# Optimization experiments

Hardware: AMD Instinct MI355X
Metric: run time of the kernel (lower is better)

Reference implementation:

```python
import jax, jax.numpy as jnp
import numpy as np

N = 100000
E = 500000
F_IN = 128
HID = 64
HEADS = 4
OUT = 32
NEG_SLOPE = 0.2


def _glorot(key, shape):
    fan_in, fan_out = shape[0], shape[1]
    lim = jnp.sqrt(6.0 / (fan_in + fan_out))
    return jax.random.uniform(key, shape, jnp.float32, -lim, lim)


def setup_inputs() -> dict:
    key = jax.random.key(0)
    ks = jax.random.split(key, 20)
    x = jax.random.normal(ks[0], (N, F_IN), jnp.float32)
    edge_index = jax.random.randint(ks[1], (2, E), 0, N, jnp.int64)
    edge_attr = jax.random.uniform(ks[2], (E, 1), jnp.float32)
    d1 = HEADS * HID
    params = {
        # conv1: F_IN -> HEADS x HID
        "Wl1": _glorot(ks[3], (F_IN, d1)), "bl1": jnp.zeros((d1,), jnp.float32),
        "Wr1": _glorot(ks[4], (F_IN, d1)), "br1": jnp.zeros((d1,), jnp.float32),
        "We1": _glorot(ks[5], (1, d1)),
        "att1": _glorot(ks[6], (HEADS, HID)),
        "b1": jnp.zeros((d1,), jnp.float32),
        "Wl2": _glorot(ks[7], (d1, OUT)), "bl2": jnp.zeros((OUT,), jnp.float32),
        "Wr2": _glorot(ks[8], (d1, OUT)), "br2": jnp.zeros((OUT,), jnp.float32),
        "We2": _glorot(ks[9], (1, OUT)),
        "att2": _glorot(ks[10], (1, OUT)),
        "b2": jnp.zeros((OUT,), jnp.float32),
    }
    return {"x": x, "edge_index": edge_index, "edge_attr": edge_attr, **params}


def gatv2_conv(x, src, dst, edge_attr, Wl, bl, Wr, br, We, att, bias, heads, out_ch):
    """PyG GATv2Conv (add_self_loops=False, concat=True, share_weights=False)."""
    n = x.shape[0]
    xl = (x @ Wl + bl).reshape(n, heads, out_ch)          # source transform
    xr = (x @ Wr + br).reshape(n, heads, out_ch)          # target transform
    e = (edge_attr @ We).reshape(-1, heads, out_ch)       # [E, H, C]
    m = jax.nn.leaky_relu(xl[src] + xr[dst] + e, NEG_SLOPE)  # [E, H, C]
    alpha = jnp.einsum('ehc,hc->eh', m, att)              # [E, H]
    # softmax over edges sharing the same destination node
    amax = jax.ops.segment_max(alpha, dst, num_segments=n)
    ealpha = jnp.exp(alpha - amax[dst])
    denom = jax.ops.segment_sum(ealpha, dst, num_segments=n)
    alpha = ealpha / (denom[dst] + 1e-16)
    out = jax.ops.segment_sum(xl[src] * alpha[:, :, None], dst, num_segments=n)
    return out.reshape(n, heads * out_ch) + bias


def reference(x, edge_index, edge_attr, Wl1, bl1, Wr1, br1, We1, att1, b1,
              Wl2, bl2, Wr2, br2, We2, att2, b2):
    src, dst = edge_index[0], edge_index[1]
    h = gatv2_conv(x, src, dst, edge_attr, Wl1, bl1, Wr1, br1, We1, att1, b1, HEADS, HID)
    h = jax.nn.relu(h)  # dropout is identity at inference
    out = gatv2_conv(h, src, dst, edge_attr, Wl2, bl2, Wr2, br2, We2, att2, b2, 1, OUT)
    return out
```

## Files before the change

### kernel.cpp

```cpp
#include <hip/hip_runtime.h>
#include <cstddef>
#include <cstdint>

#define F_IN 128
#define D1   256
#define HEADS 4
#define HID   64
#define OUT_C 32
#define NEG   0.2f

typedef unsigned short ushort_t;
typedef __attribute__((ext_vector_type(8))) short short8;
typedef __attribute__((ext_vector_type(4))) float f32x4;
typedef __attribute__((ext_vector_type(4))) unsigned short ushort4v;

__device__ __forceinline__ float bu2f(ushort_t u) {
  return __uint_as_float(((unsigned)u) << 16);
}
__device__ __forceinline__ ushort_t f2bu(float f) {
  unsigned u = __float_as_uint(f);
  return (ushort_t)((u + 0x7FFF + ((u >> 16) & 1)) >> 16);
}

__global__ void cvt_x_k(const float* __restrict__ x, ushort_t* __restrict__ xb, int total4) {
  int i = blockIdx.x * blockDim.x + threadIdx.x;
  if (i >= total4) return;
  f32x4 v = ((const f32x4*)x)[i];
  ushort4v o;
  o[0] = f2bu(v[0]); o[1] = f2bu(v[1]); o[2] = f2bu(v[2]); o[3] = f2bu(v[3]);
  *(ushort4v*)(xb + 4 * (size_t)i) = o;
}

__global__ void prep_b1_k(const float* __restrict__ Wl, const float* __restrict__ Wr,
                          const float* __restrict__ bl, const float* __restrict__ br,
                          ushort_t* __restrict__ Bt, float* __restrict__ biasc) {
  int i = blockIdx.x * blockDim.x + threadIdx.x;
  int nn = i >> 7, k = i & 127;
  float v = (nn < D1) ? Wl[(size_t)k * D1 + nn] : Wr[(size_t)k * D1 + (nn - D1)];
  Bt[(size_t)nn * F_IN + k] = f2bu(v);
  if (k == 0) biasc[nn] = (nn < D1) ? bl[nn] : br[nn - D1];
}

__global__ void prep_b2_k(const float* __restrict__ Wl, const float* __restrict__ Wr,
                          const float* __restrict__ bl, const float* __restrict__ br,
                          ushort_t* __restrict__ Bt, float* __restrict__ biasc) {
  int i = blockIdx.x * blockDim.x + threadIdx.x;
  int nn = i >> 8, k = i & 255;
  float v = (nn < OUT_C) ? Wl[(size_t)k * OUT_C + nn] : Wr[(size_t)k * OUT_C + (nn - OUT_C)];
  Bt[(size_t)nn * D1 + k] = f2bu(v);
  if (k == 0) biasc[nn] = (nn < OUT_C) ? bl[nn] : br[nn - OUT_C];
}

template <int WM, int WN, int BK>
__global__ void mfma_gemm(const ushort_t* __restrict__ A, const ushort_t* __restrict__ Bt,
                          const float* __restrict__ biasc, ushort_t* __restrict__ C,
                          int M, int N, int K) {
  constexpr int BM = WM * 64, BN = WN * 64;
  constexpr int LD = BK + 8;
  constexpr int CPR = BK / 8;
  __shared__ ushort_t As[BM][LD];
  __shared__ ushort_t Bs[BN][LD];
  const int tid = threadIdx.x;
  const int wave = tid >> 6, lane = tid & 63;
  const int wm = wave % WM, wn = wave / WM;
  const int quad = lane >> 4, l16 = lane & 15;
  const int m0 = blockIdx.x * BM, n0 = blockIdx.y * BN;
  const int nth = WM * WN * 64;
  f32x4 acc[4][4] = {};
  for (int k0 = 0; k0 < K; k0 += BK) {
    for (int i = tid; i < BM * CPR; i += nth) {
      int r = i / CPR, ch = i % CPR;
      int gr = m0 + r;
      short8 v = {};
      if (gr < M) v = *(const short8*)(A + (size_t)gr * K + k0 + ch * 8);
      *(short8*)(&As[r][ch * 8]) = v;
    }
    for (int i = tid; i < BN * CPR; i += nth) {
      int r = i / CPR, ch = i % CPR;
      short8 v = {};
      if (n0 + r < N) v = *(const short8*)(Bt + (size_t)(n0 + r) * K + k0 + ch * 8);
      *(short8*)(&Bs[r][ch * 8]) = v;
    }
    __syncthreads();
#pragma unroll
    for (int ks = 0; ks < BK; ks += 32) {
      short8 af[4], bfr[4];
#pragma unroll
      for (int mi = 0; mi < 4; ++mi)
        af[mi] = *(const short8*)(&As[wm * 64 + mi * 16 + l16][ks + quad * 8]);
#pragma unroll
      for (int ni = 0; ni < 4; ++ni)
        bfr[ni] = *(const short8*)(&Bs[wn * 64 + ni * 16 + l16][ks + quad * 8]);
#pragma unroll
      for (int mi = 0; mi < 4; ++mi)
#pragma unroll
        for (int ni = 0; ni < 4; ++ni)
          acc[mi][ni] = __builtin_amdgcn_mfma_f32_16x16x32_bf16(af[mi], bfr[ni],
                                                                acc[mi][ni], 0, 0, 0);
    }
    __syncthreads();
  }
#pragma unroll
  for (int mi = 0; mi < 4; ++mi) {
#pragma unroll
    for (int r = 0; r < 4; ++r) {
      int grow = m0 + wm * 64 + mi * 16 + quad * 4 + r;
      if (grow >= M) continue;
#pragma unroll
      for (int ni = 0; ni < 4; ++ni) {
        int gcol = n0 + wn * 64 + ni * 16 + l16;
        C[(size_t)grow * N + gcol] = f2bu(acc[mi][ni][r] + biasc[gcol]);
      }
    }
  }
}

__global__ void hist_k(const int* __restrict__ dst, int* __restrict__ deg, int e) {
  int i = blockIdx.x * blockDim.x + threadIdx.x;
  if (i < e) atomicAdd(&deg[dst[i]], 1);
}

__global__ void scan_block_k(const int* __restrict__ deg, int* __restrict__ row_ptr,
                             int* __restrict__ bsum, int n) {
  __shared__ int s[1024];
  int i = blockIdx.x * 1024 + threadIdx.x;
  int v = (i < n) ? deg[i] : 0;
  s[threadIdx.x] = v;
  __syncthreads();
  for (int off = 1; off < 1024; off <<= 1) {
    int t = (threadIdx.x >= off) ? s[threadIdx.x - off] : 0;
    __syncthreads();
    s[threadIdx.x] += t;
    __syncthreads();
  }
  if (i < n) row_ptr[i + 1] = s[threadIdx.x];
  if (threadIdx.x == 1023) bsum[blockIdx.x] = s[1023];
}

__global__ void scan_bsum_k(int* __restrict__ bsum, int nb) {
  __shared__ int s[128];
  int v = (threadIdx.x < nb) ? bsum[threadIdx.x] : 0;
  s[threadIdx.x] = v;
  __syncthreads();
  for (int off = 1; off < 128; off <<= 1) {
    int t = (threadIdx.x >= off) ? s[threadIdx.x - off] : 0;
    __syncthreads();
    s[threadIdx.x] += t;
    __syncthreads();
  }
  if (threadIdx.x < nb) bsum[threadIdx.x] = s[threadIdx.x] - v;
}

__global__ void add_off_k(int* __restrict__ row_ptr, const int* __restrict__ bsum, int n) {
  int i = blockIdx.x * blockDim.x + threadIdx.x;
  if (i == 0) row_ptr[0] = 0;
  if (i < n) row_ptr[i + 1] += bsum[i >> 10];
}

__global__ void copy_cursor_k(const int* __restrict__ row_ptr, int* __restrict__ cursor, int n) {
  int i = blockIdx.x * blockDim.x + threadIdx.x;
  if (i < n) cursor[i] = row_ptr[i];
}

__global__ void fill_k(const int* __restrict__ src, const int* __restrict__ dst,
                       const float* __restrict__ eattr, int* __restrict__ cursor,
                       int* __restrict__ csr_src, float* __restrict__ csr_w, int e) {
  int i = blockIdx.x * blockDim.x + threadIdx.x;
  if (i >= e) return;
  int p = atomicAdd(&cursor[dst[i]], 1);
  csr_src[p] = src[i];
  csr_w[p]   = eattr[i];
}

__global__ void gat1_k(const int* __restrict__ row_ptr, const int* __restrict__ csr_src,
                       const float* __restrict__ csr_w, const ushort_t* __restrict__ C1,
                       const float* __restrict__ We, const float* __restrict__ att,
                       const float* __restrict__ bias, ushort_t* __restrict__ h1, int n) {
  int node = (int)(((size_t)blockIdx.x * blockDim.x + threadIdx.x) >> 6);
  int lane = threadIdx.x & 63;
  if (node >= n) return;
  int cb = lane * 4;
  ushort4v xr4 = *(const ushort4v*)(C1 + (size_t)node * 512 + 256 + cb);
  float xrr[4], Wev[4], attv[4], acc[4] = {0.f, 0.f, 0.f, 0.f};
  float esum = 0.f;
#pragma unroll
  for (int j = 0; j < 4; ++j) {
    xrr[j] = bu2f(xr4[j]);
    Wev[j] = We[cb + j];
    attv[j] = att[cb + j];
  }
  int p1 = row_ptr[node + 1];
  for (int p = row_ptr[node]; p < p1; ++p) {
    int s = csr_src[p];
    float wgt = csr_w[p];
    ushort4v xl4 = *(const ushort4v*)(C1 + (size_t)s * 512 + cb);
    float xv[4], v = 0.f;
#pragma unroll
    for (int j = 0; j < 4; ++j) {
      xv[j] = bu2f(xl4[j]);
      float m = xv[j] + xrr[j] + wgt * Wev[j];
      m = m > 0.f ? m : NEG * m;
      v += m * attv[j];
    }
    v += __shfl_xor(v, 1, 64);
    v += __shfl_xor(v, 2, 64);
    v += __shfl_xor(v, 4, 64);
    v += __shfl_xor(v, 8, 64);
    float eh = __expf(v);
    esum += eh;
#pragma unroll
    for (int j = 0; j < 4; ++j) acc[j] += eh * xv[j];
  }
  float inv = 1.f / (esum + 1e-16f);
  ushort4v o;
#pragma unroll
  for (int j = 0; j < 4; ++j) {
    float t = acc[j] * inv + bias[cb + j];
    o[j] = f2bu(t > 0.f ? t : 0.f);
  }
  *(ushort4v*)(h1 + (size_t)node * D1 + cb) = o;
}

__global__ void gat2_k(const int* __restrict__ row_ptr, const int* __restrict__ csr_src,
                       const float* __restrict__ csr_w, const ushort_t* __restrict__ C2,
                       const float* __restrict__ We, const float* __restrict__ att,
                       const float* __restrict__ bias, float* __restrict__ out, int n) {
  size_t t = (size_t)blockIdx.x * blockDim.x + threadIdx.x;
  int node = (int)(t >> 3);
  int g = (int)(t & 7);
  if (node >= n) return;
  int cb = g * 4;
  ushort4v xr4 = *(const ushort4v*)(C2 + (size_t)node * 64 + 32 + cb);
  float xrr[4], Wev[4], attv[4], acc[4] = {0.f, 0.f, 0.f, 0.f};
  float esum = 0.f;
#pragma unroll
  for (int j = 0; j < 4; ++j) {
    xrr[j] = bu2f(xr4[j]);
    Wev[j] = We[cb + j];
    attv[j] = att[cb + j];
  }
  int p1 = row_ptr[node + 1];
  for (int p = row_ptr[node]; p < p1; ++p) {
    int s = csr_src[p];
    float wgt = csr_w[p];
    ushort4v xl4 = *(const ushort4v*)(C2 + (size_t)s * 64 + cb);
    float xv[4], v = 0.f;
#pragma unroll
    for (int j = 0; j < 4; ++j) {
      xv[j] = bu2f(xl4[j]);
      float m = xv[j] + xrr[j] + wgt * Wev[j];
      m = m > 0.f ? m : NEG * m;
      v += m * attv[j];
    }
    v += __shfl_xor(v, 1, 64);
    v += __shfl_xor(v, 2, 64);
    v += __shfl_xor(v, 4, 64);
    float eh = __expf(v);
    esum += eh;
#pragma unroll
    for (int j = 0; j < 4; ++j) acc[j] += eh * xv[j];
  }
  float inv = 1.f / (esum + 1e-16f);
  f32x4 ov;
#pragma unroll
  for (int j = 0; j < 4; ++j) ov[j] = acc[j] * inv + bias[cb + j];
  *(f32x4*)(out + (size_t)node * OUT_C + cb) = ov;
}

extern "C" void kernel_launch(void* const* d_in, const int* in_sizes, int n_in,
                              void* d_out, int out_size, void* d_ws, size_t ws_size,
                              hipStream_t stream) {
  const float* x     = (const float*)d_in[0];
  const int*   eidx  = (const int*)d_in[1];
  const float* eattr = (const float*)d_in[2];
  const float* Wl1 = (const float*)d_in[3];
  const float* bl1 = (const float*)d_in[4];
  const float* Wr1 = (const float*)d_in[5];
  const float* br1 = (const float*)d_in[6];
  const float* We1 = (const float*)d_in[7];
  const float* att1 = (const float*)d_in[8];
  const float* b1  = (const float*)d_in[9];
  const float* Wl2 = (const float*)d_in[10];
  const float* bl2 = (const float*)d_in[11];
  const float* Wr2 = (const float*)d_in[12];
  const float* br2 = (const float*)d_in[13];
  const float* We2 = (const float*)d_in[14];
  const float* att2 = (const float*)d_in[15];
  const float* b2  = (const float*)d_in[16];

  const int n = in_sizes[0] / F_IN;
  const int e = in_sizes[2];
  const int* src = eidx;
  const int* dst = eidx + e;
  float* out = (float*)d_out;

  char* w = (char*)d_ws;
  ushort_t* x_bf = (ushort_t*)w;  w += (size_t)n * F_IN * 2;
  ushort_t* C1   = (ushort_t*)w;  w += (size_t)n * 512 * 2;
  ushort_t* h1b  = (ushort_t*)w;  w += (size_t)n * D1 * 2;
  ushort_t* C2   = (ushort_t*)w;  w += (size_t)n * 64 * 2;
  ushort_t* Bt1  = (ushort_t*)w;  w += 512 * F_IN * 2;
  ushort_t* Bt2  = (ushort_t*)w;  w += 64 * D1 * 2;
  float* bias1c  = (float*)w;     w += 512 * 4;
  float* bias2c  = (float*)w;     w += 64 * 4;
  float* csr_w   = (float*)w;     w += (size_t)e * 4;
  int*   csr_src = (int*)w;       w += (size_t)e * 4;
  int*   row_ptr = (int*)w;       w += ((size_t)n + 1) * 4;
  int*   cursor  = (int*)w;       w += (size_t)n * 4;
  int*   bsum    = (int*)w;       w += 512;
  int*   deg = cursor;

  dim3 blk(256);
  const int nb = (n + 1023) / 1024;

  cvt_x_k<<<(n * F_IN / 4 + 255) / 256, blk, 0, stream>>>(x, x_bf, n * F_IN / 4);
  prep_b1_k<<<(512 * 128) / 256, blk, 0, stream>>>(Wl1, Wr1, bl1, br1, Bt1, bias1c);
  prep_b2_k<<<(64 * 256) / 256, blk, 0, stream>>>(Wl2, Wr2, bl2, br2, Bt2, bias2c);

  hipMemsetAsync(deg, 0, (size_t)n * sizeof(int), stream);
  hist_k<<<(e + 255) / 256, blk, 0, stream>>>(dst, deg, e);
  scan_block_k<<<nb, 1024, 0, stream>>>(deg, row_ptr, bsum, n);
  scan_bsum_k<<<1, 128, 0, stream>>>(bsum, nb);
  add_off_k<<<(n + 255) / 256, blk, 0, stream>>>(row_ptr, bsum, n);
  copy_cursor_k<<<(n + 255) / 256, blk, 0, stream>>>(row_ptr, cursor, n);
  fill_k<<<(e + 255) / 256, blk, 0, stream>>>(src, dst, eattr, cursor, csr_src, csr_w, e);

  mfma_gemm<2, 2, 64><<<dim3((n + 127) / 128, 4), blk, 0, stream>>>(
      x_bf, Bt1, bias1c, C1, n, 512, F_IN);
  gat1_k<<<(n + 3) / 4, blk, 0, stream>>>(row_ptr, csr_src, csr_w, C1,
                                          We1, att1, b1, h1b, n);

  mfma_gemm<4, 1, 64><<<dim3((n + 255) / 256, 1), blk, 0, stream>>>(
      h1b, Bt2, bias2c, C2, n, 64, D1);
  gat2_k<<<((size_t)n * 8 + 255) / 256, blk, 0, stream>>>(row_ptr, csr_src, csr_w, C2,
                                                          We2, att2, b2, out, n);
}
```

Before: 382.9 us.

## Fuse x conversion into GEMM, pack CSR edges, unroll gather loops, retile GEMM2

Removes the separate fp32-to-bf16 conversion kernel by converting x on the fly while loading A tiles in the first GEMM. CSR source index and edge weight are packed into a single int2 array, so each edge needs one load instead of two. The attention aggregation loops in both GAT kernels are unrolled by four to keep more independent gathers in flight. The second GEMM moves to 128-thread blocks of 128 rows for more blocks. The first GEMM now reads fp32 x, and with four column blocks per row tile it re-reads and re-converts x each time.

```diff
diff --git a/kernel.cpp b/kernel.cpp
--- a/kernel.cpp
+++ b/kernel.cpp
@@ -22,15 +22,6 @@
   return (ushort_t)((u + 0x7FFF + ((u >> 16) & 1)) >> 16);
 }
 
-__global__ void cvt_x_k(const float* __restrict__ x, ushort_t* __restrict__ xb, int total4) {
-  int i = blockIdx.x * blockDim.x + threadIdx.x;
-  if (i >= total4) return;
-  f32x4 v = ((const f32x4*)x)[i];
-  ushort4v o;
-  o[0] = f2bu(v[0]); o[1] = f2bu(v[1]); o[2] = f2bu(v[2]); o[3] = f2bu(v[3]);
-  *(ushort4v*)(xb + 4 * (size_t)i) = o;
-}
-
 __global__ void prep_b1_k(const float* __restrict__ Wl, const float* __restrict__ Wr,
                           const float* __restrict__ bl, const float* __restrict__ br,
                           ushort_t* __restrict__ Bt, float* __restrict__ biasc) {
@@ -51,8 +42,8 @@
   if (k == 0) biasc[nn] = (nn < OUT_C) ? bl[nn] : br[nn - OUT_C];
 }
 
-template <int WM, int WN, int BK>
-__global__ void mfma_gemm(const ushort_t* __restrict__ A, const ushort_t* __restrict__ Bt,
+template <int WM, int WN, int BK, bool CVT>
+__global__ void mfma_gemm(const void* __restrict__ Av, const ushort_t* __restrict__ Bt,
                           const float* __restrict__ biasc, ushort_t* __restrict__ C,
                           int M, int N, int K) {
   constexpr int BM = WM * 64, BN = WN * 64;
@@ -71,9 +62,26 @@
     for (int i = tid; i < BM * CPR; i += nth) {
       int r = i / CPR, ch = i % CPR;
       int gr = m0 + r;
-      short8 v = {};
-      if (gr < M) v = *(const short8*)(A + (size_t)gr * K + k0 + ch * 8);
-      *(short8*)(&As[r][ch * 8]) = v;
+      if (CVT) {
+        const float* A32 = (const float*)Av;
+        f32x4 v0 = {}, v1 = {};
+        if (gr < M) {
+          const float* p = A32 + (size_t)gr * K + k0 + ch * 8;
+          v0 = *(const f32x4*)p;
+          v1 = *(const f32x4*)(p + 4);
+        }
+        short8 o;
+        o[0] = (short)f2bu(v0[0]); o[1] = (short)f2bu(v0[1]);
+        o[2] = (short)f2bu(v0[2]); o[3] = (short)f2bu(v0[3]);
+        o[4] = (short)f2bu(v1[0]); o[5] = (short)f2bu(v1[1]);
+        o[6] = (short)f2bu(v1[2]); o[7] = (short)f2bu(v1[3]);
+        *(short8*)(&As[r][ch * 8]) = o;
+      } else {
+        const ushort_t* A16 = (const ushort_t*)Av;
+        short8 v = {};
+        if (gr < M) v = *(const short8*)(A16 + (size_t)gr * K + k0 + ch * 8);
+        *(short8*)(&As[r][ch * 8]) = v;
+      }
     }
     for (int i = tid; i < BN * CPR; i += nth) {
       int r = i / CPR, ch = i % CPR;
@@ -164,16 +172,15 @@
 
 __global__ void fill_k(const int* __restrict__ src, const int* __restrict__ dst,
                        const float* __restrict__ eattr, int* __restrict__ cursor,
-                       int* __restrict__ csr_src, float* __restrict__ csr_w, int e) {
+                       int2* __restrict__ csr, int e) {
   int i = blockIdx.x * blockDim.x + threadIdx.x;
   if (i >= e) return;
   int p = atomicAdd(&cursor[dst[i]], 1);
-  csr_src[p] = src[i];
-  csr_w[p]   = eattr[i];
-}
-
-__global__ void gat1_k(const int* __restrict__ row_ptr, const int* __restrict__ csr_src,
-                       const float* __restrict__ csr_w, const ushort_t* __restrict__ C1,
+  csr[p] = make_int2(src[i], __float_as_int(eattr[i]));
+}
+
+__global__ void gat1_k(const int* __restrict__ row_ptr, const int2* __restrict__ csr,
+                       const ushort_t* __restrict__ C1,
                        const float* __restrict__ We, const float* __restrict__ att,
                        const float* __restrict__ bias, ushort_t* __restrict__ h1, int n) {
   int node = (int)(((size_t)blockIdx.x * blockDim.x + threadIdx.x) >> 6);
@@ -189,11 +196,47 @@
     Wev[j] = We[cb + j];
     attv[j] = att[cb + j];
   }
-  int p1 = row_ptr[node + 1];
-  for (int p = row_ptr[node]; p < p1; ++p) {
-    int s = csr_src[p];
-    float wgt = csr_w[p];
-    ushort4v xl4 = *(const ushort4v*)(C1 + (size_t)s * 512 + cb);
+  int p = row_ptr[node], p1 = row_ptr[node + 1];
+  for (; p + 4 <= p1; p += 4) {
+    int2 ee[4];
+#pragma unroll
+    for (int u = 0; u < 4; ++u) ee[u] = csr[p + u];
+    ushort4v xl4[4];
+#pragma unroll
+    for (int u = 0; u < 4; ++u)
+      xl4[u] = *(const ushort4v*)(C1 + (size_t)ee[u].x * 512 + cb);
+    float xv[4][4], v[4];
+#pragma unroll
+    for (int u = 0; u < 4; ++u) {
+      float wgt = __int_as_float(ee[u].y);
+      v[u] = 0.f;
+#pragma unroll
+      for (int j = 0; j < 4; ++j) {
+        xv[u][j] = bu2f(xl4[u][j]);
+        float m = xv[u][j] + xrr[j] + wgt * Wev[j];
+        m = m > 0.f ? m : NEG * m;
+        v[u] += m * attv[j];
+      }
+    }
+#pragma unroll
+    for (int u = 0; u < 4; ++u) {
+      v[u] += __shfl_xor(v[u], 1, 64);
+      v[u] += __shfl_xor(v[u], 2, 64);
+      v[u] += __shfl_xor(v[u], 4, 64);
+      v[u] += __shfl_xor(v[u], 8, 64);
+    }
+#pragma unroll
+    for (int u = 0; u < 4; ++u) {
+      float eh = __expf(v[u]);
+      esum += eh;
+#pragma unroll
+      for (int j = 0; j < 4; ++j) acc[j] += eh * xv[u][j];
+    }
+  }
+  for (; p < p1; ++p) {
+    int2 ed = csr[p];
+    float wgt = __int_as_float(ed.y);
+    ushort4v xl4 = *(const ushort4v*)(C1 + (size_t)ed.x * 512 + cb);
     float xv[4], v = 0.f;
 #pragma unroll
     for (int j = 0; j < 4; ++j) {
@@ -221,8 +264,8 @@
   *(ushort4v*)(h1 + (size_t)node * D1 + cb) = o;
 }
 
-__global__ void gat2_k(const int* __restrict__ row_ptr, const int* __restrict__ csr_src,
-                       const float* __restrict__ csr_w, const ushort_t* __restrict__ C2,
+__global__ void gat2_k(const int* __restrict__ row_ptr, const int2* __restrict__ csr,
+                       const ushort_t* __restrict__ C2,
                        const float* __restrict__ We, const float* __restrict__ att,
                        const float* __restrict__ bias, float* __restrict__ out, int n) {
   size_t t = (size_t)blockIdx.x * blockDim.x + threadIdx.x;
@@ -239,11 +282,46 @@
     Wev[j] = We[cb + j];
     attv[j] = att[cb + j];
   }
-  int p1 = row_ptr[node + 1];
-  for (int p = row_ptr[node]; p < p1; ++p) {
-    int s = csr_src[p];
-    float wgt = csr_w[p];
-    ushort4v xl4 = *(const ushort4v*)(C2 + (size_t)s * 64 + cb);
+  int p = row_ptr[node], p1 = row_ptr[node + 1];
+  for (; p + 4 <= p1; p += 4) {
+    int2 ee[4];
+#pragma unroll
+    for (int u = 0; u < 4; ++u) ee[u] = csr[p + u];
+    ushort4v xl4[4];
+#pragma unroll
+    for (int u = 0; u < 4; ++u)
+      xl4[u] = *(const ushort4v*)(C2 + (size_t)ee[u].x * 64 + cb);
+    float xv[4][4], v[4];
+#pragma unroll
+    for (int u = 0; u < 4; ++u) {
+      float wgt = __int_as_float(ee[u].y);
+      v[u] = 0.f;
+#pragma unroll
+      for (int j = 0; j < 4; ++j) {
+        xv[u][j] = bu2f(xl4[u][j]);
+        float m = xv[u][j] + xrr[j] + wgt * Wev[j];
+        m = m > 0.f ? m : NEG * m;
+        v[u] += m * attv[j];
+      }
+    }
+#pragma unroll
+    for (int u = 0; u < 4; ++u) {
+      v[u] += __shfl_xor(v[u], 1, 64);
+      v[u] += __shfl_xor(v[u], 2, 64);
+      v[u] += __shfl_xor(v[u], 4, 64);
+    }
+#pragma unroll
+    for (int u = 0; u < 4; ++u) {
+      float eh = __expf(v[u]);
+      esum += eh;
+#pragma unroll
+      for (int j = 0; j < 4; ++j) acc[j] += eh * xv[u][j];
+    }
+  }
+  for (; p < p1; ++p) {
+    int2 ed = csr[p];
+    float wgt = __int_as_float(ed.y);
+    ushort4v xl4 = *(const ushort4v*)(C2 + (size_t)ed.x * 64 + cb);
     float xv[4], v = 0.f;
 #pragma unroll
     for (int j = 0; j < 4; ++j) {
@@ -295,7 +373,6 @@
   float* out = (float*)d_out;
 
   char* w = (char*)d_ws;
-  ushort_t* x_bf = (ushort_t*)w;  w += (size_t)n * F_IN * 2;
   ushort_t* C1   = (ushort_t*)w;  w += (size_t)n * 512 * 2;
   ushort_t* h1b  = (ushort_t*)w;  w += (size_t)n * D1 * 2;
   ushort_t* C2   = (ushort_t*)w;  w += (size_t)n * 64 * 2;
@@ -303,8 +380,7 @@
   ushort_t* Bt2  = (ushort_t*)w;  w += 64 * D1 * 2;
   float* bias1c  = (float*)w;     w += 512 * 4;
   float* bias2c  = (float*)w;     w += 64 * 4;
-  float* csr_w   = (float*)w;     w += (size_t)e * 4;
-  int*   csr_src = (int*)w;       w += (size_t)e * 4;
+  int2*  csr     = (int2*)w;      w += (size_t)e * 8;
   int*   row_ptr = (int*)w;       w += ((size_t)n + 1) * 4;
   int*   cursor  = (int*)w;       w += (size_t)n * 4;
   int*   bsum    = (int*)w;       w += 512;
@@ -313,7 +389,6 @@
   dim3 blk(256);
   const int nb = (n + 1023) / 1024;
 
-  cvt_x_k<<<(n * F_IN / 4 + 255) / 256, blk, 0, stream>>>(x, x_bf, n * F_IN / 4);
   prep_b1_k<<<(512 * 128) / 256, blk, 0, stream>>>(Wl1, Wr1, bl1, br1, Bt1, bias1c);
   prep_b2_k<<<(64 * 256) / 256, blk, 0, stream>>>(Wl2, Wr2, bl2, br2, Bt2, bias2c);
 
@@ -323,15 +398,14 @@
   scan_bsum_k<<<1, 128, 0, stream>>>(bsum, nb);
   add_off_k<<<(n + 255) / 256, blk, 0, stream>>>(row_ptr, bsum, n);
   copy_cursor_k<<<(n + 255) / 256, blk, 0, stream>>>(row_ptr, cursor, n);
-  fill_k<<<(e + 255) / 256, blk, 0, stream>>>(src, dst, eattr, cursor, csr_src, csr_w, e);
-
-  mfma_gemm<2, 2, 64><<<dim3((n + 127) / 128, 4), blk, 0, stream>>>(
-      x_bf, Bt1, bias1c, C1, n, 512, F_IN);
-  gat1_k<<<(n + 3) / 4, blk, 0, stream>>>(row_ptr, csr_src, csr_w, C1,
-                                          We1, att1, b1, h1b, n);
-
-  mfma_gemm<4, 1, 64><<<dim3((n + 255) / 256, 1), blk, 0, stream>>>(
+  fill_k<<<(e + 255) / 256, blk, 0, stream>>>(src, dst, eattr, cursor, csr, e);
+
+  mfma_gemm<2, 2, 64, true><<<dim3((n + 127) / 128, 4), blk, 0, stream>>>(
+      x, Bt1, bias1c, C1, n, 512, F_IN);
+  gat1_k<<<(n + 3) / 4, blk, 0, stream>>>(row_ptr, csr, C1, We1, att1, b1, h1b, n);
+
+  mfma_gemm<2, 1, 64, false><<<dim3((n + 127) / 128, 1), dim3(128), 0, stream>>>(
       h1b, Bt2, bias2c, C2, n, 64, D1);
-  gat2_k<<<((size_t)n * 8 + 255) / 256, blk, 0, stream>>>(row_ptr, csr_src, csr_w, C2,
+  gat2_k<<<((size_t)n * 8 + 255) / 256, blk, 0, stream>>>(row_ptr, csr, C2,
                                                           We2, att2, b2, out, n);
 }
```

Result: faster. 353.2 us (-7.8%).
